# Kernel optimization log

Hardware: AMD Instinct MI355X
Metric: run time of the kernel (lower is better)

Reference implementation:

```python
import jax, jax.numpy as jnp
import numpy as np

LAYER_SPECS = [(2, 4, 1), (2, 4, 1), (1, 4, 1), (1, 4, 1)]
SKIPS = [(k - s) * d for (s, k, d) in LAYER_SPECS]  # (ksz-stride)*dilation
C = 80  # encoder channels


def _conv1d(x, w, b, stride, dilation):
    # x: (N, Cin, L), w: (Cout, Cin, K)
    out = jax.lax.conv_general_dilated(
        x, w, window_strides=(stride,), padding='VALID',
        rhs_dilation=(dilation,), dimension_numbers=('NCH', 'OIH', 'NCH'))
    return out + b[None, :, None]


def _encoder(x, w_wide, b_wide, w_1x1, b_1x1, w_f0, b_f0, w_f1, b_f1):
    # x: (N, T, 80) -> (N, T', 80)
    x = jnp.transpose(x, (0, 2, 1))  # (N, 80, T)
    for i, ((stride, ksz, dil), skip) in enumerate(zip(LAYER_SPECS, SKIPS)):
        x1 = _conv1d(x, w_wide[i], b_wide[i], stride, dil)  # (N, 2C, L')
        a, g = jnp.split(x1, 2, axis=1)
        x2 = jnp.tanh(a) * jax.nn.sigmoid(g)                # gated activation
        x3 = _conv1d(x2, w_1x1[i], b_1x1[i], 1, 1)          # (N, C, L')
        if i == 0:
            x = x3
        else:
            T3 = x3.shape[2]
            # residual: strided slice of previous x, take last of each stride group
            res = x[:, :, skip:skip + T3 * stride].reshape(x.shape[0], C, T3, stride)[:, :, :, -1]
            x = x3 + res
    x = _conv1d(jax.nn.relu(_conv1d(x, w_f0, b_f0, 1, 1)), w_f1, b_f1, 1, 1)
    return jnp.transpose(x, (0, 2, 1))  # (N, T', 80)


def setup_inputs() -> dict:
    key = jax.random.key(0)
    ks = jax.random.split(key, 10)
    N, Ts, Tq = 16, 8192, 2048
    return {
        'search': jax.random.normal(ks[0], (N, Ts, 80), dtype=jnp.float32),
        'query': jax.random.normal(ks[1], (N, Tq, 80), dtype=jnp.float32),
        'w_wide': jax.random.normal(ks[2], (4, 160, 80, 4), dtype=jnp.float32) * 0.02,
        'b_wide': jnp.zeros((4, 160), dtype=jnp.float32),
        'w_1x1': jax.random.normal(ks[3], (4, 80, 80, 1), dtype=jnp.float32) * 0.05,
        'b_1x1': jnp.zeros((4, 80), dtype=jnp.float32),
        'w_f0': jax.random.normal(ks[4], (80, 80, 1), dtype=jnp.float32) * 0.05,
        'b_f0': jnp.zeros((80,), dtype=jnp.float32),
        'w_f1': jax.random.normal(ks[5], (80, 80, 1), dtype=jnp.float32) * 0.05,
        'b_f1': jax.random.normal(ks[6], (80,), dtype=jnp.float32) * 0.05,
        'embedding': jax.random.normal(ks[7], (1, 512, 80), dtype=jnp.float32) * 0.001,
        'w_lin': jax.random.normal(ks[8], (2, 80), dtype=jnp.float32) * 0.05,
        'b_lin': jnp.zeros((2,), dtype=jnp.float32),
    }


def reference(search, query, w_wide, b_wide, w_1x1, b_1x1,
              w_f0, b_f0, w_f1, b_f1, embedding, w_lin, b_lin):
    enc_s = _encoder(search, w_wide, b_wide, w_1x1, b_1x1, w_f0, b_f0, w_f1, b_f1)
    enc_q = _encoder(query, w_wide, b_wide, w_1x1, b_1x1, w_f0, b_f0, w_f1, b_f1)

    # ---- VectorQuant (no normalize): nearest-codeword lookup + straight-through ----
    x = enc_s[:, :, None, :]                  # (N, T, 1, V)
    N, T, nc, V = x.shape
    n_classes = embedding.shape[1]
    x1 = x.reshape(N * T, nc, V)              # (NT, 1, V)
    # squared-distance via expansion: argmin identical to argmin of L2 norm
    x2 = jnp.sum(x1 * x1, axis=-1, keepdims=True)          # (NT, 1, 1)
    e2 = jnp.sum(embedding * embedding, axis=-1)[None]     # (1, 1, K)
    xe = jnp.einsum('ncv,ckv->nck', x1, embedding)         # (NT, 1, K)
    idx = jnp.argmin(x2 - 2.0 * xe + e2, axis=2)           # (NT, 1)
    offset = jnp.arange(nc) * n_classes
    flat = embedding.reshape(-1, V)
    output = flat[(idx + offset[None, :]).reshape(-1)].reshape(x.shape)
    out0 = jax.lax.stop_gradient(output - x) + x           # straight-through
    discrete = out0[:, :, 0, :]               # (N, Ts', V)

    # ---- align query to search length, classify, max-pool over time ----
    sf = discrete.shape[1] // enc_q.shape[1]
    q = jnp.tile(enc_q, (1, sf, 1))
    pad = discrete.shape[1] - q.shape[1]
    q = jnp.pad(q, ((0, 0), (0, pad), (0, 0)))
    pred = jnp.tanh((q + discrete) @ w_lin.T + b_lin)      # (N, Ts', 2)
    return jnp.max(pred, axis=1)                           # (N, 2)
```

## Files before the change

kernel.cpp:

```cpp
#include <hip/hip_runtime.h>
#include <math.h>


#define NBATCH 16

typedef __attribute__((ext_vector_type(8))) short s16x8;
typedef __attribute__((ext_vector_type(4))) float f32x4;

__device__ __forceinline__ float fast_sigmoid(float x){ return 1.0f/(1.0f+__expf(-x)); }
__device__ __forceinline__ float fast_tanh(float x){ return 2.0f/(1.0f+__expf(-2.0f*x))-1.0f; }
__device__ __forceinline__ unsigned short f2bf(float f){
    unsigned int u = __float_as_uint(f);
    return (unsigned short)((u + 0x7FFFu + ((u >> 16) & 1u)) >> 16);
}
__device__ __forceinline__ unsigned int pk2bf(float lo, float hi){
    unsigned int r;
    asm("v_cvt_pk_bf16_f32 %0, %1, %2" : "=v"(r) : "v"(lo), "v"(hi));
    return r;
}
__device__ __forceinline__ unsigned short cvt1bf(float v){
    return (unsigned short)pk2bf(v, v);
}

__global__ __launch_bounds__(256) void pack_all(
    const float* __restrict__ w_wide, const float* __restrict__ w_1x1,
    const float* __restrict__ wf0,    const float* __restrict__ wf1,
    const float* __restrict__ emb,
    unsigned short* __restrict__ WW, unsigned short* __restrict__ W1,
    unsigned short* __restrict__ F0, unsigned short* __restrict__ F1,
    unsigned short* __restrict__ EM, float* __restrict__ e2o)
{
    int i = blockIdx.x * 256 + threadIdx.x;
    if (i < 204800) {
        int l = i / 51200, r = i % 51200, oc = r / 320, k = r % 320;
        int j = k / 80, ic = k % 80;
        WW[i] = f2bf(w_wide[l * 51200 + oc * 320 + ic * 4 + j]);
    } else if (i < 235520) {
        int idx = i - 204800, l = idx / 7680, r = idx % 7680, oc = r / 96, k = r % 96;
        W1[idx] = (k < 80) ? f2bf(w_1x1[l * 6400 + oc * 80 + k]) : (unsigned short)0;
    } else if (i < 243200) {
        int idx = i - 235520, oc = idx / 96, k = idx % 96;
        F0[idx] = (k < 80) ? f2bf(wf0[oc * 80 + k]) : (unsigned short)0;
    } else if (i < 250880) {
        int idx = i - 243200, oc = idx / 96, k = idx % 96;
        F1[idx] = (k < 80) ? f2bf(wf1[oc * 80 + k]) : (unsigned short)0;
    } else if (i < 291840) {
        EM[i - 250880] = f2bf(emb[i - 250880]);
    } else if (i < 292352) {
        int e = i - 291840;
        float s = 0.f;
        for (int k = 0; k < 80; ++k) { float v = emb[e * 80 + k]; s = fmaf(v, v, s); }
        e2o[e] = s;
    }
}

template<int S, bool HAS_RES, bool FINAL>
__global__ __launch_bounds__(320, 3) void enc_layer(
    const float* __restrict__ xS, const float* __restrict__ xQ,
    const unsigned short* __restrict__ ww,  const float* __restrict__ wb,
    const unsigned short* __restrict__ w1p, const float* __restrict__ b1,
    const unsigned short* __restrict__ f0p, const float* __restrict__ bf0,
    const unsigned short* __restrict__ f1p, const float* __restrict__ bf1,
    float* __restrict__ outS, float* __restrict__ outQ,
    int TinS, int ToutS, int TinQ, int ToutQ, int nbS)
{
    constexpr int MT   = 4;
    constexpr int P    = 63 * S + 4;
    constexpr int HALF = (S == 2) ? 65 : 67;
    constexpr int NPARY= (S == 2) ? 2 : 1;
    constexpr int NEL  = P * 20;
    constexpr int NST  = (NEL + 319) / 320;

    __shared__ __attribute__((aligned(16))) unsigned short xs[NPARY * HALF * 88];
    __shared__ __attribute__((aligned(16))) unsigned short gsA[64 * 104];
    __shared__ __attribute__((aligned(16))) unsigned short gsB[FINAL ? 64 * 104 : 8];

    const int tid  = threadIdx.x;
    const int wave = tid >> 6;
    const int lane = tid & 63;
    const int m    = lane & 15;
    const int quad = lane >> 4;
    const int quad8 = quad * 8;
    const int c    = wave * 16 + m;
    const int n_   = blockIdx.y;

    const float* x; float* out; int T_in, T_out, bx;
    if ((int)blockIdx.x < nbS) { x = xS; out = outS; T_in = TinS; T_out = ToutS; bx = blockIdx.x; }
    else                       { x = xQ; out = outQ; T_in = TinQ; T_out = ToutQ; bx = blockIdx.x - nbS; }
    const int t0 = bx * 64;
    const long base_in = (long)n_ * T_in * 80;

    float4 vst[NST]; int odx[NST]; bool okw[NST];
#pragma unroll
    for (int it = 0; it < NST; ++it) {
        int u = tid + it * 320;
        okw[it] = (u < NEL);
        if (u >= NEL) u = NEL - 1;
        int pos = u / 20, c4 = u % 20;
        int tp = t0 * S + pos; if (tp > T_in - 1) tp = T_in - 1;
        vst[it] = *(const float4*)(x + base_in + (long)tp * 80 + c4 * 4);
        int row = (S == 2) ? (pos >> 1) : pos;
        int par = (S == 2) ? (pos & 1) : 0;
        odx[it] = (par * HALF + row) * 88 + c4 * 4;
    }

    const unsigned short* wa_base = ww + (long)c * 320 + quad8;
    const unsigned short* wg_base = ww + (long)(80 + c) * 320 + quad8;
    s16x8 baP[3], bgP[3];
    baP[0] = *(const s16x8*)(wa_base);       bgP[0] = *(const s16x8*)(wg_base);
    baP[1] = *(const s16x8*)(wa_base + 32);  bgP[1] = *(const s16x8*)(wg_base + 32);

    const unsigned short* wb1 = w1p + (long)c * 96 + quad8;
    s16x8 w1b0 = *(const s16x8*)(wb1);
    s16x8 w1b1 = *(const s16x8*)(wb1 + 32);
    s16x8 w1b2 = *(const s16x8*)(wb1 + 64);

    float resv[16];
    if (HAS_RES) {
#pragma unroll
        for (int mt = 0; mt < MT; ++mt)
#pragma unroll
            for (int r = 0; r < 4; ++r) {
                int tg = t0 + mt * 16 + quad * 4 + r;
                if (tg > T_out - 1) tg = T_out - 1;
                resv[mt * 4 + r] = x[base_in + (long)(3 + (long)tg * S) * 80 + c];
            }
    }

#pragma unroll
    for (int it = 0; it < NST; ++it) {
        if (okw[it]) {
            float4 v = vst[it];
            *(uint2*)&xs[odx[it]] = make_uint2(pk2bf(v.x, v.y), pk2bf(v.z, v.w));
        }
    }

    f32x4 acc_a[MT], acc_g[MT];
#pragma unroll
    for (int mt = 0; mt < MT; ++mt) {
        acc_a[mt] = (f32x4){0.f, 0.f, 0.f, 0.f};
        acc_g[mt] = (f32x4){0.f, 0.f, 0.f, 0.f};
    }

    __syncthreads();

#pragma unroll
    for (int kk = 0; kk < 10; ++kk) {
        if (kk + 2 < 10) {
            baP[(kk + 2) % 3] = *(const s16x8*)(wa_base + (kk + 2) * 32);
            bgP[(kk + 2) % 3] = *(const s16x8*)(wg_base + (kk + 2) * 32);
        }
        const int kq = kk * 32 + quad8;
        const int j  = (kq >= 240) ? 3 : ((kq >= 160) ? 2 : ((kq >= 80) ? 1 : 0));
        const int ic0 = kq - j * 80;
        int xb;
        if (S == 2) xb = ((j & 1) * HALF + (j >> 1)) * 88 + ic0;
        else        xb = j * 88 + ic0;
        s16x8 a[MT];
#pragma unroll
        for (int mt = 0; mt < MT; ++mt)
            a[mt] = *(const s16x8*)&xs[xb + (mt * 16 + m) * 88];
        s16x8 ba = baP[kk % 3], bg = bgP[kk % 3];
#pragma unroll
        for (int mt = 0; mt < MT; ++mt) {
            acc_a[mt] = __builtin_amdgcn_mfma_f32_16x16x32_bf16(a[mt], ba, acc_a[mt], 0, 0, 0);
            acc_g[mt] = __builtin_amdgcn_mfma_f32_16x16x32_bf16(a[mt], bg, acc_g[mt], 0, 0, 0);
        }
    }

    const float ba_b = wb[c];
    const float bg_b = wb[80 + c];
#pragma unroll
    for (int mt = 0; mt < MT; ++mt)
#pragma unroll
        for (int r = 0; r < 4; ++r) {
            float av = acc_a[mt][r] + ba_b;
            float gv = acc_g[mt][r] + bg_b;
            gsA[(mt * 16 + quad * 4 + r) * 104 + c] =
                cvt1bf(fast_tanh(av) * fast_sigmoid(gv));
        }
    const uint4 z4 = make_uint4(0u, 0u, 0u, 0u);
    {
        constexpr int NPAD = FINAL ? 256 : 128;
        for (int u = tid; u < NPAD; u += 320) {
            unsigned short* g = (u < 128) ? gsA : gsB;
            int v = u & 127;
            *(uint4*)&g[(v >> 1) * 104 + 80 + (v & 1) * 8] = z4;
        }
    }
    __syncthreads();

    auto mm96 = [&](s16x8 b0, s16x8 b1f, s16x8 b2, const unsigned short* g, f32x4 (&o)[MT]) {
#pragma unroll
        for (int mt = 0; mt < MT; ++mt) o[mt] = (f32x4){0.f, 0.f, 0.f, 0.f};
#pragma unroll
        for (int kb = 0; kb < 3; ++kb) {
            s16x8 b = (kb == 0) ? b0 : ((kb == 1) ? b1f : b2);
#pragma unroll
            for (int mt = 0; mt < MT; ++mt) {
                s16x8 ag = *(const s16x8*)&g[(mt * 16 + m) * 104 + kb * 32 + quad8];
                o[mt] = __builtin_amdgcn_mfma_f32_16x16x32_bf16(ag, b, o[mt], 0, 0, 0);
            }
        }
    };

    f32x4 a1[MT];
    mm96(w1b0, w1b1, w1b2, gsA, a1);

    const long base_out = (long)n_ * T_out * 80;
    const float b1c = b1[c];
    if (!FINAL) {
#pragma unroll
        for (int mt = 0; mt < MT; ++mt)
#pragma unroll
            for (int r = 0; r < 4; ++r) {
                int tg = t0 + mt * 16 + quad * 4 + r;
                if (tg < T_out) {
                    float v = a1[mt][r] + b1c;
                    if (HAS_RES) v += resv[mt * 4 + r];
                    out[base_out + (long)tg * 80 + c] = v;
                }
            }
    } else {
        float x3[MT][4];
#pragma unroll
        for (int mt = 0; mt < MT; ++mt)
#pragma unroll
            for (int r = 0; r < 4; ++r) {
                float v = a1[mt][r] + b1c;
                if (HAS_RES) v += resv[mt * 4 + r];
                x3[mt][r] = v;
            }
        const unsigned short* wf0b = f0p + (long)c * 96 + quad8;
        s16x8 f0b0 = *(const s16x8*)(wf0b);
        s16x8 f0b1 = *(const s16x8*)(wf0b + 32);
        s16x8 f0b2 = *(const s16x8*)(wf0b + 64);
        const float bf0c = bf0[c];
#pragma unroll
        for (int mt = 0; mt < MT; ++mt)
#pragma unroll
            for (int r = 0; r < 4; ++r)
                gsB[(mt * 16 + quad * 4 + r) * 104 + c] = cvt1bf(x3[mt][r]);
        __syncthreads();
        f32x4 a2[MT];
        mm96(f0b0, f0b1, f0b2, gsB, a2);
        const unsigned short* wf1b = f1p + (long)c * 96 + quad8;
        s16x8 f1b0 = *(const s16x8*)(wf1b);
        s16x8 f1b1 = *(const s16x8*)(wf1b + 32);
        s16x8 f1b2 = *(const s16x8*)(wf1b + 64);
        const float bf1c = bf1[c];
#pragma unroll
        for (int mt = 0; mt < MT; ++mt)
#pragma unroll
            for (int r = 0; r < 4; ++r)
                gsA[(mt * 16 + quad * 4 + r) * 104 + c] =
                    cvt1bf(fmaxf(a2[mt][r] + bf0c, 0.f));
        __syncthreads();
        f32x4 a3[MT];
        mm96(f1b0, f1b1, f1b2, gsA, a3);
#pragma unroll
        for (int mt = 0; mt < MT; ++mt)
#pragma unroll
            for (int r = 0; r < 4; ++r) {
                int tg = t0 + mt * 16 + quad * 4 + r;
                if (tg < T_out)
                    out[base_out + (long)tg * 80 + c] = a3[mt][r] + bf1c;
            }
    }
}

__global__ __launch_bounds__(256, 2) void vq_mfma(
    const float* __restrict__ enc_s, const float* __restrict__ enc_q,
    const unsigned short* __restrict__ embp, const float* __restrict__ emb,
    const float* __restrict__ e2v,
    const float* __restrict__ w_lin, const float* __restrict__ b_lin,
    float* __restrict__ pred)
{
    __shared__ unsigned short xs[64 * 104];
    __shared__ unsigned short es[128 * 104];
    const uint4 z4 = make_uint4(0u, 0u, 0u, 0u);

    const int tid  = threadIdx.x;
    const int wave = tid >> 6;
    const int lane = tid & 63;
    const int m    = lane & 15;
    const int quad = lane >> 4;
    const int n    = blockIdx.y;
    const int t0   = blockIdx.x * 64;

    for (int u = tid; u < 64 * 20; u += 256) {
        int row = u / 20, c4 = u % 20;
        int t = t0 + row; if (t > 2039) t = 2039;
        float4 v = *(const float4*)(enc_s + ((long)n * 2040 + t) * 80 + c4 * 4);
        *(uint2*)&xs[row * 104 + c4 * 4] = make_uint2(pk2bf(v.x, v.y), pk2bf(v.z, v.w));
    }
    for (int u = tid; u < 128; u += 256)
        *(uint4*)&xs[(u >> 1) * 104 + 80 + (u & 1) * 8] = z4;
    __syncthreads();

    s16x8 af[3];
#pragma unroll
    for (int kb = 0; kb < 3; ++kb)
        af[kb] = *(const s16x8*)&xs[(wave * 16 + m) * 104 + kb * 32 + quad * 8];

    float best[4]; int bi[4];
#pragma unroll
    for (int r = 0; r < 4; ++r) { best[r] = 1e30f; bi[r] = 0; }

    for (int ch = 0; ch < 4; ++ch) {
        const int c0 = ch * 128;
        __syncthreads();
        for (int u = tid; u < 128 * 12; u += 256) {
            int el = u / 12, seg = u % 12;
            uint4 v = z4;
            if (seg < 10) v = *(const uint4*)(embp + (long)(c0 + el) * 80 + seg * 8);
            *(uint4*)&es[el * 104 + seg * 8] = v;
        }
        __syncthreads();

        f32x4 acc[8];
#pragma unroll
        for (int nt = 0; nt < 8; ++nt) acc[nt] = (f32x4){0.f, 0.f, 0.f, 0.f};
#pragma unroll
        for (int kb = 0; kb < 3; ++kb) {
            const int k0 = kb * 32 + quad * 8;
#pragma unroll
            for (int nt = 0; nt < 8; ++nt) {
                s16x8 b = *(const s16x8*)&es[(nt * 16 + m) * 104 + k0];
                acc[nt] = __builtin_amdgcn_mfma_f32_16x16x32_bf16(af[kb], b, acc[nt], 0, 0, 0);
            }
        }
#pragma unroll
        for (int nt = 0; nt < 8; ++nt) {
            const int e = c0 + nt * 16 + m;
            const float e2x = e2v[e];
#pragma unroll
            for (int r = 0; r < 4; ++r) {
                float s = fmaf(-2.0f, acc[nt][r], e2x);
                if (s < best[r]) { best[r] = s; bi[r] = e; }
            }
        }
    }

    __syncthreads();
    float* rb  = (float*)es;
    int*   ri  = (int*)es + 1088;
    float* rb2 = (float*)es + 2176;
    int*   ri2 = (int*)es + 2432;
#pragma unroll
    for (int r = 0; r < 4; ++r) {
        int tl = wave * 16 + quad * 4 + r;
        rb[tl * 17 + m] = best[r];
        ri[tl * 17 + m] = bi[r];
    }
    __syncthreads();

    {
        const int t = tid >> 2, g = tid & 3;
        const int o = t * 17 + g * 4;
        float b = rb[o]; int ix = ri[o];
#pragma unroll
        for (int j = 1; j < 4; ++j) {
            float v = rb[o + j]; int iv = ri[o + j];
            if (v < b || (v == b && iv < ix)) { b = v; ix = iv; }
        }
        rb2[t * 4 + g] = b; ri2[t * 4 + g] = ix;
    }
    __syncthreads();

    if (tid < 128) {
        const int trow = tid >> 1, h = tid & 1;
        float b = rb2[trow * 4]; int ix = ri2[trow * 4];
#pragma unroll
        for (int j = 1; j < 4; ++j) {
            float v = rb2[trow * 4 + j]; int iv = ri2[trow * 4 + j];
            if (v < b || (v == b && iv < ix)) { b = v; ix = iv; }
        }
        const int t = t0 + trow;
        if (t < 2040) {
            const float4* ev = (const float4*)(emb + (long)ix * 80);
            const bool hasq = (t < 2016);
            const float4* qv = hasq
                ? (const float4*)(enc_q + ((long)n * 504 + (t % 504)) * 80) : nullptr;
            const float4* wl = (const float4*)(w_lin + h * 80);
            float p = b_lin[h];
#pragma unroll
            for (int i = 0; i < 20; ++i) {
                float4 e4 = ev[i];
                float4 q4 = hasq ? qv[i] : make_float4(0.f, 0.f, 0.f, 0.f);
                float4 w4 = wl[i];
                p = fmaf(e4.x + q4.x, w4.x, p);
                p = fmaf(e4.y + q4.y, w4.y, p);
                p = fmaf(e4.z + q4.z, w4.z, p);
                p = fmaf(e4.w + q4.w, w4.w, p);
            }
            pred[((long)n * 2040 + t) * 2 + h] = fast_tanh(p);
        }
    }
}

__global__ __launch_bounds__(256) void max_red(const float* __restrict__ pred,
                                               float* __restrict__ out)
{
    __shared__ float s0[256], s1[256];
    const int n = blockIdx.x, tid = threadIdx.x;
    float m0 = -1e30f, m1 = -1e30f;
    for (int t = tid; t < 2040; t += 256) {
        long o = ((long)n * 2040 + t) * 2;
        m0 = fmaxf(m0, pred[o]);
        m1 = fmaxf(m1, pred[o + 1]);
    }
    s0[tid] = m0; s1[tid] = m1;
    __syncthreads();
    for (int st = 128; st > 0; st >>= 1) {
        if (tid < st) {
            s0[tid] = fmaxf(s0[tid], s0[tid + st]);
            s1[tid] = fmaxf(s1[tid], s1[tid + st]);
        }
        __syncthreads();
    }
    if (tid == 0) { out[n * 2] = s0[0]; out[n * 2 + 1] = s1[0]; }
}

extern "C" void kernel_launch(void* const* d_in, const int* in_sizes, int n_in,
                              void* d_out, int out_size, void* d_ws, size_t ws_size,
                              hipStream_t stream)
{
    const float* search = (const float*)d_in[0];
    const float* query  = (const float*)d_in[1];
    const float* w_wide = (const float*)d_in[2];
    const float* b_wide = (const float*)d_in[3];
    const float* w_1x1  = (const float*)d_in[4];
    const float* b_1x1  = (const float*)d_in[5];
    const float* w_f0   = (const float*)d_in[6];
    const float* b_f0   = (const float*)d_in[7];
    const float* w_f1   = (const float*)d_in[8];
    const float* b_f1   = (const float*)d_in[9];
    const float* emb    = (const float*)d_in[10];
    const float* w_lin  = (const float*)d_in[11];
    const float* b_lin  = (const float*)d_in[12];
    float* out = (float*)d_out;
    float* ws  = (float*)d_ws;

    float* A  = ws;
    float* B  = A  + 5241600;
    float* C  = B  + 2618880;
    float* QA = C  + 2618880;
    float* QB = QA + 1309440;
    float* QC = QB + 652800;
    unsigned short* WWp = (unsigned short*)(QC + 652800);
    unsigned short* W1p = WWp + 204800;
    unsigned short* F0p = W1p + 30720;
    unsigned short* F1p = F0p + 7680;
    unsigned short* EMp = F1p + 7680;
    float* e2b = (float*)(EMp + 40960);

    const dim3 blk(320);
    auto nb = [](int T) { return (T + 63) / 64; };

    pack_all<<<dim3(1142), dim3(256), 0, stream>>>(w_wide, w_1x1, w_f0, w_f1, emb,
                                                   WWp, W1p, F0p, F1p, EMp, e2b);

    enc_layer<2, false, false><<<dim3(nb(4095) + nb(1023), NBATCH), blk, 0, stream>>>(
        search, query, WWp, b_wide, W1p, b_1x1, nullptr, nullptr, nullptr, nullptr,
        A, QA, 8192, 4095, 2048, 1023, nb(4095));
    enc_layer<2, true, false><<<dim3(nb(2046) + nb(510), NBATCH), blk, 0, stream>>>(
        A, QA, WWp + 51200, b_wide + 160, W1p + 7680, b_1x1 + 80,
        nullptr, nullptr, nullptr, nullptr,
        B, QB, 4095, 2046, 1023, 510, nb(2046));
    enc_layer<1, true, false><<<dim3(nb(2043) + nb(507), NBATCH), blk, 0, stream>>>(
        B, QB, WWp + 102400, b_wide + 320, W1p + 15360, b_1x1 + 160,
        nullptr, nullptr, nullptr, nullptr,
        C, QC, 2046, 2043, 510, 507, nb(2043));
    enc_layer<1, true, true><<<dim3(nb(2040) + nb(504), NBATCH), blk, 0, stream>>>(
        C, QC, WWp + 153600, b_wide + 480, W1p + 23040, b_1x1 + 240,
        F0p, b_f0, F1p, b_f1,
        B, QB, 2043, 2040, 507, 504, nb(2040));

    vq_mfma<<<dim3(32, NBATCH), dim3(256), 0, stream>>>(B, QB, EMp, emb, e2b,
                                                        w_lin, b_lin, C);
    max_red<<<dim3(NBATCH), dim3(256), 0, stream>>>(C, out);
}
```

Measured before the change: 254.3 us.

## Fuse encoder layers 1-3 and final 1x1 convs into one halo-tiled kernel

Replaces three separate encoder-layer launches with one kernel. For each 64-step output tile it loads a 142-row input halo and runs layers 1-3 plus the two final 1x1 convs entirely in LDS, keeping intermediates and residuals in bf16 shared memory. This removes the global round trips and launch gaps between layers. In exchange it recomputes halo rows (80-row tiles for 64 outputs), uses much more LDS (about 70 KB, occupancy bound lowered to 2), and rounds residuals to bf16. The VQ argmin reduction is also restructured into a single 64-thread pass that computes both linear outputs per thread, and its input conversion switches to software bf16 rounding.

```diff
diff --git a/kernel.cpp b/kernel.cpp
--- a/kernel.cpp
+++ b/kernel.cpp
@@ -20,6 +20,9 @@
 }
 __device__ __forceinline__ unsigned short cvt1bf(float v){
     return (unsigned short)pk2bf(v, v);
+}
+__device__ __forceinline__ float bf2f(unsigned short s){
+    return __uint_as_float(((unsigned int)s) << 16);
 }
 
 __global__ __launch_bounds__(256) void pack_all(
@@ -59,8 +62,6 @@
     const float* __restrict__ xS, const float* __restrict__ xQ,
     const unsigned short* __restrict__ ww,  const float* __restrict__ wb,
     const unsigned short* __restrict__ w1p, const float* __restrict__ b1,
-    const unsigned short* __restrict__ f0p, const float* __restrict__ bf0,
-    const unsigned short* __restrict__ f1p, const float* __restrict__ bf1,
     float* __restrict__ outS, float* __restrict__ outQ,
     int TinS, int ToutS, int TinQ, int ToutQ, int nbS)
 {
@@ -73,7 +74,6 @@
 
     __shared__ __attribute__((aligned(16))) unsigned short xs[NPARY * HALF * 88];
     __shared__ __attribute__((aligned(16))) unsigned short gsA[64 * 104];
-    __shared__ __attribute__((aligned(16))) unsigned short gsB[FINAL ? 64 * 104 : 8];
 
     const int tid  = threadIdx.x;
     const int wave = tid >> 6;
@@ -115,18 +115,6 @@
     s16x8 w1b1 = *(const s16x8*)(wb1 + 32);
     s16x8 w1b2 = *(const s16x8*)(wb1 + 64);
 
-    float resv[16];
-    if (HAS_RES) {
-#pragma unroll
-        for (int mt = 0; mt < MT; ++mt)
-#pragma unroll
-            for (int r = 0; r < 4; ++r) {
-                int tg = t0 + mt * 16 + quad * 4 + r;
-                if (tg > T_out - 1) tg = T_out - 1;
-                resv[mt * 4 + r] = x[base_in + (long)(3 + (long)tg * S) * 80 + c];
-            }
-    }
-
 #pragma unroll
     for (int it = 0; it < NST; ++it) {
         if (okw[it]) {
@@ -180,91 +168,326 @@
                 cvt1bf(fast_tanh(av) * fast_sigmoid(gv));
         }
     const uint4 z4 = make_uint4(0u, 0u, 0u, 0u);
-    {
-        constexpr int NPAD = FINAL ? 256 : 128;
-        for (int u = tid; u < NPAD; u += 320) {
-            unsigned short* g = (u < 128) ? gsA : gsB;
-            int v = u & 127;
-            *(uint4*)&g[(v >> 1) * 104 + 80 + (v & 1) * 8] = z4;
-        }
-    }
-    __syncthreads();
-
-    auto mm96 = [&](s16x8 b0, s16x8 b1f, s16x8 b2, const unsigned short* g, f32x4 (&o)[MT]) {
-#pragma unroll
-        for (int mt = 0; mt < MT; ++mt) o[mt] = (f32x4){0.f, 0.f, 0.f, 0.f};
+    for (int u = tid; u < 128; u += 320)
+        *(uint4*)&gsA[(u >> 1) * 104 + 80 + (u & 1) * 8] = z4;
+    __syncthreads();
+
+    f32x4 a1[MT];
+#pragma unroll
+    for (int mt = 0; mt < MT; ++mt) a1[mt] = (f32x4){0.f, 0.f, 0.f, 0.f};
+#pragma unroll
+    for (int kb = 0; kb < 3; ++kb) {
+        s16x8 b = (kb == 0) ? w1b0 : ((kb == 1) ? w1b1 : w1b2);
+#pragma unroll
+        for (int mt = 0; mt < MT; ++mt) {
+            s16x8 ag = *(const s16x8*)&gsA[(mt * 16 + m) * 104 + kb * 32 + quad8];
+            a1[mt] = __builtin_amdgcn_mfma_f32_16x16x32_bf16(ag, b, a1[mt], 0, 0, 0);
+        }
+    }
+
+    const long base_out = (long)n_ * T_out * 80;
+    const float b1c = b1[c];
+#pragma unroll
+    for (int mt = 0; mt < MT; ++mt)
+#pragma unroll
+        for (int r = 0; r < 4; ++r) {
+            int tg = t0 + mt * 16 + quad * 4 + r;
+            if (tg < T_out)
+                out[base_out + (long)tg * 80 + c] = a1[mt][r] + b1c;
+        }
+}
+
+__global__ __launch_bounds__(320, 2) void enc_fuse123(
+    const float* __restrict__ xS, const float* __restrict__ xQ,
+    const unsigned short* __restrict__ WW, const float* __restrict__ WB,
+    const unsigned short* __restrict__ W1, const float* __restrict__ BB1,
+    const unsigned short* __restrict__ F0p, const float* __restrict__ BF0,
+    const unsigned short* __restrict__ F1p, const float* __restrict__ BF1,
+    float* __restrict__ outS, float* __restrict__ outQ,
+    int TinS, int ToutS, int TinQ, int ToutQ, int nbS)
+{
+    constexpr int AOFF = 0, B1OFF = 12496, B2OFF = 19776, GOFF = 26744;
+    constexpr int NEL = 142 * 20, NST = 9;
+    __shared__ __attribute__((aligned(16))) unsigned short Ld[35064];
+
+    const int tid  = threadIdx.x;
+    const int wave = tid >> 6;
+    const int lane = tid & 63;
+    const int m    = lane & 15;
+    const int quad = lane >> 4;
+    const int quad8 = quad * 8;
+    const int c    = wave * 16 + m;
+    const int n_   = blockIdx.y;
+
+    const float* x; float* out; int TinA, Tout, bx;
+    if ((int)blockIdx.x < nbS) { x = xS; out = outS; TinA = TinS; Tout = ToutS; bx = blockIdx.x; }
+    else                       { x = xQ; out = outQ; TinA = TinQ; Tout = ToutQ; bx = blockIdx.x - nbS; }
+    const int t0 = bx * 64;
+    const long base_in = (long)n_ * TinA * 80;
+    const long base_out = (long)n_ * Tout * 80;
+
+    float4 vst[NST]; int odx[NST]; bool okw[NST];
+#pragma unroll
+    for (int it = 0; it < NST; ++it) {
+        int u = tid + it * 320;
+        okw[it] = (u < NEL);
+        if (u >= NEL) u = NEL - 1;
+        int pos = u / 20, c4 = u % 20;
+        int ra = 2 * t0 + pos; if (ra > TinA - 1) ra = TinA - 1;
+        vst[it] = *(const float4*)(x + base_in + (long)ra * 80 + c4 * 4);
+        odx[it] = ((pos & 1) * 71 + (pos >> 1)) * 88 + c4 * 4;
+    }
+
+    const unsigned short* wa1 = WW + 51200 + (long)c * 320 + quad8;
+    const unsigned short* wg1 = WW + 51200 + (long)(80 + c) * 320 + quad8;
+    s16x8 baP[3], bgP[3];
+    baP[0] = *(const s16x8*)(wa1);       bgP[0] = *(const s16x8*)(wg1);
+    baP[1] = *(const s16x8*)(wa1 + 32);  bgP[1] = *(const s16x8*)(wg1 + 32);
+    const unsigned short* w1l1 = W1 + 7680 + (long)c * 96 + quad8;
+    s16x8 wA0 = *(const s16x8*)(w1l1);
+    s16x8 wA1 = *(const s16x8*)(w1l1 + 32);
+    s16x8 wA2 = *(const s16x8*)(w1l1 + 64);
+
+#pragma unroll
+    for (int it = 0; it < NST; ++it) {
+        if (okw[it]) {
+            float4 v = vst[it];
+            *(uint2*)&Ld[AOFF + odx[it]] = make_uint2(pk2bf(v.x, v.y), pk2bf(v.z, v.w));
+        }
+    }
+    const uint4 z4 = make_uint4(0u, 0u, 0u, 0u);
+    for (int u = tid; u < 160; u += 320)
+        *(uint4*)&Ld[GOFF + (u >> 1) * 104 + 80 + (u & 1) * 8] = z4;
+
+    f32x4 aa[5], ag[5];
+#pragma unroll
+    for (int mt = 0; mt < 5; ++mt) {
+        aa[mt] = (f32x4){0.f, 0.f, 0.f, 0.f};
+        ag[mt] = (f32x4){0.f, 0.f, 0.f, 0.f};
+    }
+    __syncthreads();
+
+    auto mm96 = [&](s16x8 b0, s16x8 b1f, s16x8 b2, int goff, f32x4 (&o)[5]) {
+#pragma unroll
+        for (int mt = 0; mt < 5; ++mt) o[mt] = (f32x4){0.f, 0.f, 0.f, 0.f};
 #pragma unroll
         for (int kb = 0; kb < 3; ++kb) {
             s16x8 b = (kb == 0) ? b0 : ((kb == 1) ? b1f : b2);
 #pragma unroll
-            for (int mt = 0; mt < MT; ++mt) {
-                s16x8 ag = *(const s16x8*)&g[(mt * 16 + m) * 104 + kb * 32 + quad8];
-                o[mt] = __builtin_amdgcn_mfma_f32_16x16x32_bf16(ag, b, o[mt], 0, 0, 0);
+            for (int mt = 0; mt < 5; ++mt) {
+                s16x8 agf = *(const s16x8*)&Ld[goff + (mt * 16 + m) * 104 + kb * 32 + quad8];
+                o[mt] = __builtin_amdgcn_mfma_f32_16x16x32_bf16(agf, b, o[mt], 0, 0, 0);
             }
         }
     };
 
-    f32x4 a1[MT];
-    mm96(w1b0, w1b1, w1b2, gsA, a1);
-
-    const long base_out = (long)n_ * T_out * 80;
-    const float b1c = b1[c];
-    if (!FINAL) {
-#pragma unroll
-        for (int mt = 0; mt < MT; ++mt)
+#pragma unroll
+    for (int kk = 0; kk < 10; ++kk) {
+        if (kk + 2 < 10) {
+            baP[(kk + 2) % 3] = *(const s16x8*)(wa1 + (kk + 2) * 32);
+            bgP[(kk + 2) % 3] = *(const s16x8*)(wg1 + (kk + 2) * 32);
+        }
+        const int kq = kk * 32 + quad8;
+        const int j  = (kq >= 240) ? 3 : ((kq >= 160) ? 2 : ((kq >= 80) ? 1 : 0));
+        const int ic0 = kq - j * 80;
+        const int xb = (j & 1) * 6248 + (j >> 1) * 88 + ic0;
+        s16x8 a[5];
+#pragma unroll
+        for (int mt = 0; mt < 5; ++mt)
+            a[mt] = *(const s16x8*)&Ld[AOFF + xb + (mt * 16 + m) * 88];
+        s16x8 ba = baP[kk % 3], bg = bgP[kk % 3];
+#pragma unroll
+        for (int mt = 0; mt < 5; ++mt) {
+            aa[mt] = __builtin_amdgcn_mfma_f32_16x16x32_bf16(a[mt], ba, aa[mt], 0, 0, 0);
+            ag[mt] = __builtin_amdgcn_mfma_f32_16x16x32_bf16(a[mt], bg, ag[mt], 0, 0, 0);
+        }
+    }
+    {
+        const float bab = WB[160 + c], bgb = WB[160 + 80 + c];
+#pragma unroll
+        for (int mt = 0; mt < 5; ++mt)
+#pragma unroll
+            for (int r = 0; r < 4; ++r) {
+                int row = mt * 16 + quad * 4 + r;
+                float av = aa[mt][r] + bab, gv = ag[mt][r] + bgb;
+                Ld[GOFF + row * 104 + c] = cvt1bf(fast_tanh(av) * fast_sigmoid(gv));
+            }
+    }
+    __syncthreads();
+    {
+        f32x4 o[5];
+        mm96(wA0, wA1, wA2, GOFF, o);
+        const float b1c = BB1[80 + c];
+#pragma unroll
+        for (int mt = 0; mt < 5; ++mt)
+#pragma unroll
+            for (int r = 0; r < 4; ++r) {
+                int row = mt * 16 + quad * 4 + r;
+                if (row < 70) {
+                    float res = bf2f(Ld[AOFF + 6248 + (row + 1) * 88 + c]);
+                    Ld[B1OFF + row * 104 + c] = cvt1bf(o[mt][r] + b1c + res);
+                }
+            }
+    }
+    const unsigned short* wa2 = WW + 102400 + (long)c * 320 + quad8;
+    const unsigned short* wg2 = WW + 102400 + (long)(80 + c) * 320 + quad8;
+    baP[0] = *(const s16x8*)(wa2);       bgP[0] = *(const s16x8*)(wg2);
+    baP[1] = *(const s16x8*)(wa2 + 32);  bgP[1] = *(const s16x8*)(wg2 + 32);
+    const unsigned short* w1l2 = W1 + 15360 + (long)c * 96 + quad8;
+    wA0 = *(const s16x8*)(w1l2);
+    wA1 = *(const s16x8*)(w1l2 + 32);
+    wA2 = *(const s16x8*)(w1l2 + 64);
+    __syncthreads();
+
+#pragma unroll
+    for (int mt = 0; mt < 5; ++mt) {
+        aa[mt] = (f32x4){0.f, 0.f, 0.f, 0.f};
+        ag[mt] = (f32x4){0.f, 0.f, 0.f, 0.f};
+    }
+#pragma unroll
+    for (int kk = 0; kk < 10; ++kk) {
+        if (kk + 2 < 10) {
+            baP[(kk + 2) % 3] = *(const s16x8*)(wa2 + (kk + 2) * 32);
+            bgP[(kk + 2) % 3] = *(const s16x8*)(wg2 + (kk + 2) * 32);
+        }
+        const int kq = kk * 32 + quad8;
+        const int j  = (kq >= 240) ? 3 : ((kq >= 160) ? 2 : ((kq >= 80) ? 1 : 0));
+        const int ic0 = kq - j * 80;
+        const int xb = j * 104 + ic0;
+        s16x8 a[5];
+#pragma unroll
+        for (int mt = 0; mt < 5; ++mt)
+            a[mt] = *(const s16x8*)&Ld[B1OFF + xb + (mt * 16 + m) * 104];
+        s16x8 ba = baP[kk % 3], bg = bgP[kk % 3];
+#pragma unroll
+        for (int mt = 0; mt < 5; ++mt) {
+            aa[mt] = __builtin_amdgcn_mfma_f32_16x16x32_bf16(a[mt], ba, aa[mt], 0, 0, 0);
+            ag[mt] = __builtin_amdgcn_mfma_f32_16x16x32_bf16(a[mt], bg, ag[mt], 0, 0, 0);
+        }
+    }
+    {
+        const float bab = WB[320 + c], bgb = WB[320 + 80 + c];
+#pragma unroll
+        for (int mt = 0; mt < 5; ++mt)
+#pragma unroll
+            for (int r = 0; r < 4; ++r) {
+                int row = mt * 16 + quad * 4 + r;
+                float av = aa[mt][r] + bab, gv = ag[mt][r] + bgb;
+                Ld[GOFF + row * 104 + c] = cvt1bf(fast_tanh(av) * fast_sigmoid(gv));
+            }
+    }
+    __syncthreads();
+    {
+        f32x4 o[5];
+        mm96(wA0, wA1, wA2, GOFF, o);
+        const float b1c = BB1[160 + c];
+#pragma unroll
+        for (int mt = 0; mt < 5; ++mt)
+#pragma unroll
+            for (int r = 0; r < 4; ++r) {
+                int row = mt * 16 + quad * 4 + r;
+                if (row < 67) {
+                    float res = bf2f(Ld[B1OFF + (row + 3) * 104 + c]);
+                    Ld[B2OFF + row * 104 + c] = cvt1bf(o[mt][r] + b1c + res);
+                }
+            }
+    }
+    const unsigned short* wa3 = WW + 153600 + (long)c * 320 + quad8;
+    const unsigned short* wg3 = WW + 153600 + (long)(80 + c) * 320 + quad8;
+    baP[0] = *(const s16x8*)(wa3);       bgP[0] = *(const s16x8*)(wg3);
+    baP[1] = *(const s16x8*)(wa3 + 32);  bgP[1] = *(const s16x8*)(wg3 + 32);
+    const unsigned short* w1l3 = W1 + 23040 + (long)c * 96 + quad8;
+    wA0 = *(const s16x8*)(w1l3);
+    wA1 = *(const s16x8*)(w1l3 + 32);
+    wA2 = *(const s16x8*)(w1l3 + 64);
+    __syncthreads();
+
+#pragma unroll
+    for (int mt = 0; mt < 5; ++mt) {
+        aa[mt] = (f32x4){0.f, 0.f, 0.f, 0.f};
+        ag[mt] = (f32x4){0.f, 0.f, 0.f, 0.f};
+    }
+#pragma unroll
+    for (int kk = 0; kk < 10; ++kk) {
+        if (kk + 2 < 10) {
+            baP[(kk + 2) % 3] = *(const s16x8*)(wa3 + (kk + 2) * 32);
+            bgP[(kk + 2) % 3] = *(const s16x8*)(wg3 + (kk + 2) * 32);
+        }
+        const int kq = kk * 32 + quad8;
+        const int j  = (kq >= 240) ? 3 : ((kq >= 160) ? 2 : ((kq >= 80) ? 1 : 0));
+        const int ic0 = kq - j * 80;
+        const int xb = j * 104 + ic0;
+        s16x8 a[5];
+#pragma unroll
+        for (int mt = 0; mt < 5; ++mt)
+            a[mt] = *(const s16x8*)&Ld[B2OFF + xb + (mt * 16 + m) * 104];
+        s16x8 ba = baP[kk % 3], bg = bgP[kk % 3];
+#pragma unroll
+        for (int mt = 0; mt < 5; ++mt) {
+            aa[mt] = __builtin_amdgcn_mfma_f32_16x16x32_bf16(a[mt], ba, aa[mt], 0, 0, 0);
+            ag[mt] = __builtin_amdgcn_mfma_f32_16x16x32_bf16(a[mt], bg, ag[mt], 0, 0, 0);
+        }
+    }
+    {
+        const float bab = WB[480 + c], bgb = WB[480 + 80 + c];
+#pragma unroll
+        for (int mt = 0; mt < 5; ++mt)
+#pragma unroll
+            for (int r = 0; r < 4; ++r) {
+                int row = mt * 16 + quad * 4 + r;
+                float av = aa[mt][r] + bab, gv = ag[mt][r] + bgb;
+                Ld[GOFF + row * 104 + c] = cvt1bf(fast_tanh(av) * fast_sigmoid(gv));
+            }
+    }
+    for (int u = tid; u < 160; u += 320)
+        *(uint4*)&Ld[AOFF + (u >> 1) * 104 + 80 + (u & 1) * 8] = z4;
+    __syncthreads();
+    {
+        f32x4 o[5];
+        mm96(wA0, wA1, wA2, GOFF, o);
+        const float b1c = BB1[240 + c];
+#pragma unroll
+        for (int mt = 0; mt < 5; ++mt)
+#pragma unroll
+            for (int r = 0; r < 4; ++r) {
+                int row = mt * 16 + quad * 4 + r;
+                float res = bf2f(Ld[B2OFF + (row + 3) * 104 + c]);
+                Ld[AOFF + row * 104 + c] = cvt1bf(o[mt][r] + b1c + res);
+            }
+    }
+    const unsigned short* wf0b = F0p + (long)c * 96 + quad8;
+    s16x8 f0b0 = *(const s16x8*)(wf0b);
+    s16x8 f0b1 = *(const s16x8*)(wf0b + 32);
+    s16x8 f0b2 = *(const s16x8*)(wf0b + 64);
+    __syncthreads();
+    {
+        f32x4 o[5];
+        mm96(f0b0, f0b1, f0b2, AOFF, o);
+        const float bf0c = BF0[c];
+#pragma unroll
+        for (int mt = 0; mt < 5; ++mt)
+#pragma unroll
+            for (int r = 0; r < 4; ++r) {
+                int row = mt * 16 + quad * 4 + r;
+                Ld[GOFF + row * 104 + c] = cvt1bf(fmaxf(o[mt][r] + bf0c, 0.f));
+            }
+    }
+    const unsigned short* wf1b = F1p + (long)c * 96 + quad8;
+    s16x8 f1b0 = *(const s16x8*)(wf1b);
+    s16x8 f1b1 = *(const s16x8*)(wf1b + 32);
+    s16x8 f1b2 = *(const s16x8*)(wf1b + 64);
+    __syncthreads();
+    {
+        f32x4 o[5];
+        mm96(f1b0, f1b1, f1b2, GOFF, o);
+        const float bf1c = BF1[c];
+#pragma unroll
+        for (int mt = 0; mt < 4; ++mt)
 #pragma unroll
             for (int r = 0; r < 4; ++r) {
                 int tg = t0 + mt * 16 + quad * 4 + r;
-                if (tg < T_out) {
-                    float v = a1[mt][r] + b1c;
-                    if (HAS_RES) v += resv[mt * 4 + r];
-                    out[base_out + (long)tg * 80 + c] = v;
-                }
-            }
-    } else {
-        float x3[MT][4];
-#pragma unroll
-        for (int mt = 0; mt < MT; ++mt)
-#pragma unroll
-            for (int r = 0; r < 4; ++r) {
-                float v = a1[mt][r] + b1c;
-                if (HAS_RES) v += resv[mt * 4 + r];
-                x3[mt][r] = v;
-            }
-        const unsigned short* wf0b = f0p + (long)c * 96 + quad8;
-        s16x8 f0b0 = *(const s16x8*)(wf0b);
-        s16x8 f0b1 = *(const s16x8*)(wf0b + 32);
-        s16x8 f0b2 = *(const s16x8*)(wf0b + 64);
-        const float bf0c = bf0[c];
-#pragma unroll
-        for (int mt = 0; mt < MT; ++mt)
-#pragma unroll
-            for (int r = 0; r < 4; ++r)
-                gsB[(mt * 16 + quad * 4 + r) * 104 + c] = cvt1bf(x3[mt][r]);
-        __syncthreads();
-        f32x4 a2[MT];
-        mm96(f0b0, f0b1, f0b2, gsB, a2);
-        const unsigned short* wf1b = f1p + (long)c * 96 + quad8;
-        s16x8 f1b0 = *(const s16x8*)(wf1b);
-        s16x8 f1b1 = *(const s16x8*)(wf1b + 32);
-        s16x8 f1b2 = *(const s16x8*)(wf1b + 64);
-        const float bf1c = bf1[c];
-#pragma unroll
-        for (int mt = 0; mt < MT; ++mt)
-#pragma unroll
-            for (int r = 0; r < 4; ++r)
-                gsA[(mt * 16 + quad * 4 + r) * 104 + c] =
-                    cvt1bf(fmaxf(a2[mt][r] + bf0c, 0.f));
-        __syncthreads();
-        f32x4 a3[MT];
-        mm96(f1b0, f1b1, f1b2, gsA, a3);
-#pragma unroll
-        for (int mt = 0; mt < MT; ++mt)
-#pragma unroll
-            for (int r = 0; r < 4; ++r) {
-                int tg = t0 + mt * 16 + quad * 4 + r;
-                if (tg < T_out)
-                    out[base_out + (long)tg * 80 + c] = a3[mt][r] + bf1c;
+                if (tg < Tout)
+                    out[base_out + (long)tg * 80 + c] = o[mt][r] + bf1c;
             }
     }
 }
@@ -292,7 +515,9 @@
         int row = u / 20, c4 = u % 20;
         int t = t0 + row; if (t > 2039) t = 2039;
         float4 v = *(const float4*)(enc_s + ((long)n * 2040 + t) * 80 + c4 * 4);
-        *(uint2*)&xs[row * 104 + c4 * 4] = make_uint2(pk2bf(v.x, v.y), pk2bf(v.z, v.w));
+        unsigned int s0 = (unsigned int)f2bf(v.x) | ((unsigned int)f2bf(v.y) << 16);
+        unsigned int s1 = (unsigned int)f2bf(v.z) | ((unsigned int)f2bf(v.w) << 16);
+        *(uint2*)&xs[row * 104 + c4 * 4] = make_uint2(s0, s1);
     }
     for (int u = tid; u < 128; u += 256)
         *(uint4*)&xs[(u >> 1) * 104 + 80 + (u & 1) * 8] = z4;
@@ -343,10 +568,8 @@
     }
 
     __syncthreads();
-    float* rb  = (float*)es;
-    int*   ri  = (int*)es + 1088;
-    float* rb2 = (float*)es + 2176;
-    int*   ri2 = (int*)es + 2432;
+    float* rb = (float*)es;
+    int*   ri = (int*)es + 1088;
 #pragma unroll
     for (int r = 0; r < 4; ++r) {
         int tl = wave * 16 + quad * 4 + r;
@@ -355,46 +578,36 @@
     }
     __syncthreads();
 
-    {
-        const int t = tid >> 2, g = tid & 3;
-        const int o = t * 17 + g * 4;
-        float b = rb[o]; int ix = ri[o];
-#pragma unroll
-        for (int j = 1; j < 4; ++j) {
-            float v = rb[o + j]; int iv = ri[o + j];
+    if (tid < 64) {
+        const int t = t0 + tid;
+        float b = rb[tid * 17]; int ix = ri[tid * 17];
+#pragma unroll
+        for (int j = 1; j < 16; ++j) {
+            float v = rb[tid * 17 + j]; int iv = ri[tid * 17 + j];
             if (v < b || (v == b && iv < ix)) { b = v; ix = iv; }
         }
-        rb2[t * 4 + g] = b; ri2[t * 4 + g] = ix;
-    }
-    __syncthreads();
-
-    if (tid < 128) {
-        const int trow = tid >> 1, h = tid & 1;
-        float b = rb2[trow * 4]; int ix = ri2[trow * 4];
-#pragma unroll
-        for (int j = 1; j < 4; ++j) {
-            float v = rb2[trow * 4 + j]; int iv = ri2[trow * 4 + j];
-            if (v < b || (v == b && iv < ix)) { b = v; ix = iv; }
-        }
-        const int t = t0 + trow;
         if (t < 2040) {
             const float4* ev = (const float4*)(emb + (long)ix * 80);
             const bool hasq = (t < 2016);
             const float4* qv = hasq
                 ? (const float4*)(enc_q + ((long)n * 504 + (t % 504)) * 80) : nullptr;
-            const float4* wl = (const float4*)(w_lin + h * 80);
-            float p = b_lin[h];
+            float p0 = b_lin[0], p1 = b_lin[1];
 #pragma unroll
             for (int i = 0; i < 20; ++i) {
                 float4 e4 = ev[i];
                 float4 q4 = hasq ? qv[i] : make_float4(0.f, 0.f, 0.f, 0.f);
-                float4 w4 = wl[i];
-                p = fmaf(e4.x + q4.x, w4.x, p);
-                p = fmaf(e4.y + q4.y, w4.y, p);
-                p = fmaf(e4.z + q4.z, w4.z, p);
-                p = fmaf(e4.w + q4.w, w4.w, p);
-            }
-            pred[((long)n * 2040 + t) * 2 + h] = fast_tanh(p);
+                float4 w0 = *(const float4*)(w_lin + 4 * i);
+                float4 w1 = *(const float4*)(w_lin + 80 + 4 * i);
+                float sx = e4.x + q4.x, sy = e4.y + q4.y;
+                float sz = e4.z + q4.z, sw = e4.w + q4.w;
+                p0 = fmaf(sx, w0.x, p0); p1 = fmaf(sx, w1.x, p1);
+                p0 = fmaf(sy, w0.y, p0); p1 = fmaf(sy, w1.y, p1);
+                p0 = fmaf(sz, w0.z, p0); p1 = fmaf(sz, w1.z, p1);
+                p0 = fmaf(sw, w0.w, p0); p1 = fmaf(sw, w1.w, p1);
+            }
+            long o = ((long)n * 2040 + t) * 2;
+            pred[o]     = fast_tanh(p0);
+            pred[o + 1] = fast_tanh(p1);
         }
     }
 }
@@ -462,20 +675,12 @@
                                                    WWp, W1p, F0p, F1p, EMp, e2b);
 
     enc_layer<2, false, false><<<dim3(nb(4095) + nb(1023), NBATCH), blk, 0, stream>>>(
-        search, query, WWp, b_wide, W1p, b_1x1, nullptr, nullptr, nullptr, nullptr,
+        search, query, WWp, b_wide, W1p, b_1x1,
         A, QA, 8192, 4095, 2048, 1023, nb(4095));
-    enc_layer<2, true, false><<<dim3(nb(2046) + nb(510), NBATCH), blk, 0, stream>>>(
-        A, QA, WWp + 51200, b_wide + 160, W1p + 7680, b_1x1 + 80,
-        nullptr, nullptr, nullptr, nullptr,
-        B, QB, 4095, 2046, 1023, 510, nb(2046));
-    enc_layer<1, true, false><<<dim3(nb(2043) + nb(507), NBATCH), blk, 0, stream>>>(
-        B, QB, WWp + 102400, b_wide + 320, W1p + 15360, b_1x1 + 160,
-        nullptr, nullptr, nullptr, nullptr,
-        C, QC, 2046, 2043, 510, 507, nb(2043));
-    enc_layer<1, true, true><<<dim3(nb(2040) + nb(504), NBATCH), blk, 0, stream>>>(
-        C, QC, WWp + 153600, b_wide + 480, W1p + 23040, b_1x1 + 240,
-        F0p, b_f0, F1p, b_f1,
-        B, QB, 2043, 2040, 507, 504, nb(2040));
+
+    enc_fuse123<<<dim3(nb(2040) + nb(504), NBATCH), blk, 0, stream>>>(
+        A, QA, WWp, b_wide, W1p, b_1x1, F0p, b_f0, F1p, b_f1,
+        B, QB, 4095, 2040, 1023, 504, nb(2040));
 
     vq_mfma<<<dim3(32, NBATCH), dim3(256), 0, stream>>>(B, QB, EMp, emb, e2b,
                                                         w_lin, b_lin, C);
```

After: 242.4 us. -4.7%, faster.
